# Optimization experiments

Measured on AMD Instinct MI355X. Metric: run time of the kernel, lower is better.

## Reference

```python
import jax, jax.numpy as jnp
import numpy as np

N, E = 50000, 800000
NODE_DIM, EDGE_DIM = 96, 64
IN_DIM = 2 * NODE_DIM + EDGE_DIM  # 256


def setup_inputs() -> dict:
    key = jax.random.key(0)
    k = jax.random.split(key, 7)
    h = jax.random.normal(k[0], (N, NODE_DIM), dtype=jnp.float32)
    edge_index = jax.random.randint(k[1], (2, E), 0, N, dtype=jnp.int64)
    edge_attr = jax.random.normal(k[2], (E, EDGE_DIM), dtype=jnp.float32)
    # Linear params (PyTorch default-ish scale)
    s = 1.0 / np.sqrt(IN_DIM)
    W_e = jax.random.uniform(k[3], (IN_DIM, NODE_DIM), jnp.float32, -s, s)
    b_e = jax.random.uniform(k[4], (NODE_DIM,), jnp.float32, -s, s)
    W_n = jax.random.uniform(k[5], (IN_DIM, NODE_DIM), jnp.float32, -s, s)
    b_n = jax.random.uniform(k[6], (NODE_DIM,), jnp.float32, -s, s)
    return {"h": h, "edge_index": edge_index, "edge_attr": edge_attr,
            "W_e": W_e, "b_e": b_e, "W_n": W_n, "b_n": b_n}


def reference(h, edge_index, edge_attr, W_e, b_e, W_n, b_n):
    src, dst = edge_index[0], edge_index[1]
    concat = jnp.concatenate([h[src], h[dst], edge_attr], axis=-1)  # [E, 256]
    gates = jax.nn.sigmoid(concat @ W_e + b_e)                      # [E, node_dim]
    messages = jax.nn.softplus(concat @ W_n + b_n)                  # [E, node_dim]
    gated = gates * messages
    n = h.shape[0]
    h_new = jax.ops.segment_sum(gated, dst, num_segments=n)         # [N, node_dim]
    edge_count = jax.ops.segment_sum(jnp.ones((dst.shape[0],), h.dtype), dst, num_segments=n)
    edge_count = jnp.clip(edge_count, 1.0, None)[:, None]
    return h + h_new / edge_count
```

## Files before the change

kernel.cpp:

```cpp
#include <hip/hip_runtime.h>
#include <hip/hip_bf16.h>


#define NODE_DIM 96
#define EDGE_DIM 64
#define IN_DIM   256
#define NT_TILES 12
#define KT_TILES 8

typedef float  f32x4  __attribute__((ext_vector_type(4)));
typedef __bf16 bf16x8 __attribute__((ext_vector_type(8)));

__device__ __forceinline__ unsigned short bf16rne(float f) {
    unsigned int u = __float_as_uint(f);
    u += 0x7FFFu + ((u >> 16) & 1u);
    return (unsigned short)(u >> 16);
}

__global__ void pack_w_kernel(const float* __restrict__ We,
                              const float* __restrict__ Wn,
                              unsigned short* __restrict__ bpack) {
    int t = blockIdx.x * blockDim.x + threadIdx.x;
    if (t >= KT_TILES * NT_TILES * 64) return;
    int tile = t >> 6, lane = t & 63;
    int kt = tile / NT_TILES, nt = tile % NT_TILES;
    const float* W = (nt < 6) ? We : Wn;
    int n  = (nt % 6) * 16 + (lane & 15);
    int k0 = kt * 32 + (lane >> 4) * 8;
    union { unsigned short u[8]; uint4 v; } tmp;
#pragma unroll
    for (int j = 0; j < 8; ++j) tmp.u[j] = bf16rne(W[(k0 + j) * NODE_DIM + n]);
    *(uint4*)(bpack + (size_t)t * 8) = tmp.v;
}

__global__ void cvt_h_kernel(const float* __restrict__ h,
                             unsigned short* __restrict__ hb, int total8) {
    int i = blockIdx.x * 256 + threadIdx.x;
    if (i >= total8) return;
    const float4 v0 = ((const float4*)h)[i * 2];
    const float4 v1 = ((const float4*)h)[i * 2 + 1];
    union { unsigned short u[8]; uint4 v; } p;
    p.u[0] = bf16rne(v0.x); p.u[1] = bf16rne(v0.y);
    p.u[2] = bf16rne(v0.z); p.u[3] = bf16rne(v0.w);
    p.u[4] = bf16rne(v1.x); p.u[5] = bf16rne(v1.y);
    p.u[6] = bf16rne(v1.z); p.u[7] = bf16rne(v1.w);
    ((uint4*)hb)[i] = p.v;
}

__global__ void hist_kernel(const int* __restrict__ eidx, unsigned* __restrict__ deg, int E) {
    int e = blockIdx.x * 256 + threadIdx.x;
    if (e < E) atomicAdd(deg + eidx[E + e], 1u);
}

__device__ __forceinline__ unsigned block_excl_scan_256(unsigned v, int tid,
                                                        unsigned* wsum, unsigned* wpre,
                                                        unsigned* total) {
    int lane = tid & 63, w = tid >> 6;
    unsigned inc = v;
#pragma unroll
    for (int o = 1; o < 64; o <<= 1) {
        unsigned t = __shfl_up(inc, o, 64);
        if (lane >= o) inc += t;
    }
    if (lane == 63) wsum[w] = inc;
    __syncthreads();
    if (tid == 0) {
        unsigned s = 0;
#pragma unroll
        for (int k = 0; k < 4; ++k) { wpre[k] = s; s += wsum[k]; }
        *total = s;
    }
    __syncthreads();
    return inc - v + wpre[w];
}

__global__ void scan_block_kernel(const unsigned* __restrict__ deg,
                                  unsigned* __restrict__ scanned,
                                  unsigned* __restrict__ blocksum, int N) {
    __shared__ unsigned wsum[4], wpre[4], total;
    int tid = threadIdx.x;
    int i = blockIdx.x * 256 + tid;
    unsigned v = (i < N) ? deg[i] : 0u;
    unsigned excl = block_excl_scan_256(v, tid, wsum, wpre, &total);
    if (i < N) scanned[i] = excl;
    if (tid == 0) blocksum[blockIdx.x] = total;
}

__global__ void scan_sums_kernel(const unsigned* __restrict__ blocksum,
                                 unsigned* __restrict__ blockpref, int NB) {
    __shared__ unsigned wsum[4], wpre[4], total;
    int tid = threadIdx.x;
    unsigned v = (tid < NB) ? blocksum[tid] : 0u;
    unsigned excl = block_excl_scan_256(v, tid, wsum, wpre, &total);
    if (tid < NB) blockpref[tid] = excl;
}

__global__ void scan_finalize_kernel(const unsigned* __restrict__ scanned,
                                     const unsigned* __restrict__ blockpref,
                                     unsigned* __restrict__ offsets,
                                     unsigned* __restrict__ cursor, int N, int E) {
    int i = blockIdx.x * 256 + threadIdx.x;
    if (i < N) {
        unsigned o = scanned[i] + blockpref[i >> 8];
        offsets[i] = o;
        cursor[i]  = o;
    }
    if (i == 0) offsets[N] = (unsigned)E;
}

__global__ void scatter_kernel(const int* __restrict__ eidx,
                               unsigned* __restrict__ cursor,
                               unsigned* __restrict__ rank, int E) {
    int e = blockIdx.x * 256 + threadIdx.x;
    if (e < E) {
        int d = eidx[E + e];
        rank[e] = atomicAdd(cursor + d, 1u);
    }
}

__global__ __launch_bounds__(256, 2)
void gemm_msg_kernel(const unsigned short* __restrict__ hb,
                     const int*   __restrict__ eidx,
                     const float* __restrict__ ea,
                     const unsigned short* __restrict__ bpack,
                     const float* __restrict__ be,
                     const float* __restrict__ bn,
                     const unsigned* __restrict__ rank,
                     unsigned short* __restrict__ msg,
                     int E) {
    const int tid  = threadIdx.x;
    const int wave = tid >> 6, lane = tid & 63;
    const int m    = lane & 15;
    const int quad = lane >> 4;
    const int base = blockIdx.x * 128 + wave * 32;

    const unsigned short* hsq[2];
    const unsigned short* hdq[2];
    const float*          epq[2];
#pragma unroll
    for (int mt = 0; mt < 2; ++mt) {
        int e  = base + mt * 16 + m;
        int eg = (e < E) ? e : (E - 1);
        int src = eidx[eg];
        int dst = eidx[E + eg];
        hsq[mt] = hb + (size_t)src * NODE_DIM + quad * 8;
        hdq[mt] = hb + (size_t)dst * NODE_DIM + quad * 8;
        epq[mt] = ea + (size_t)eg  * EDGE_DIM + quad * 8;
    }

    unsigned prow_[2][4];
#pragma unroll
    for (int mt = 0; mt < 2; ++mt)
#pragma unroll
        for (int r = 0; r < 4; ++r) {
            int ee = base + mt * 16 + quad * 4 + r;
            prow_[mt][r] = rank[(ee < E) ? ee : (E - 1)];
        }

    float bev[6], bnv[6];
#pragma unroll
    for (int nt = 0; nt < 6; ++nt) {
        bev[nt] = be[nt * 16 + m];
        bnv[nt] = bn[nt * 16 + m];
    }

    bf16x8 A[2][KT_TILES];
#pragma unroll
    for (int mt = 0; mt < 2; ++mt) {
#pragma unroll
        for (int kt = 0; kt < 3; ++kt)
            A[mt][kt] = *(const bf16x8*)(hsq[mt] + kt * 32);
#pragma unroll
        for (int kt = 3; kt < 6; ++kt)
            A[mt][kt] = *(const bf16x8*)(hdq[mt] + (kt - 3) * 32);
#pragma unroll
        for (int kt = 6; kt < 8; ++kt) {
            const float4 v0 = *(const float4*)(epq[mt] + (kt - 6) * 32);
            const float4 v1 = *(const float4*)(epq[mt] + (kt - 6) * 32 + 4);
            union { unsigned short u[8]; bf16x8 b; } t;
            t.u[0] = bf16rne(v0.x); t.u[1] = bf16rne(v0.y);
            t.u[2] = bf16rne(v0.z); t.u[3] = bf16rne(v0.w);
            t.u[4] = bf16rne(v1.x); t.u[5] = bf16rne(v1.y);
            t.u[6] = bf16rne(v1.z); t.u[7] = bf16rne(v1.w);
            A[mt][kt] = t.b;
        }
    }

    f32x4 acc[2][NT_TILES];
#pragma unroll
    for (int mt = 0; mt < 2; ++mt)
#pragma unroll
        for (int nt = 0; nt < NT_TILES; ++nt) acc[mt][nt] = (f32x4){0.f, 0.f, 0.f, 0.f};

    const unsigned short* bl = bpack + lane * 8;
#pragma unroll
    for (int kt = 0; kt < KT_TILES; ++kt) {
        bf16x8 Bf[NT_TILES];
#pragma unroll
        for (int nt = 0; nt < NT_TILES; ++nt)
            Bf[nt] = *(const bf16x8*)(bl + (kt * NT_TILES + nt) * 512);
#pragma unroll
        for (int nt = 0; nt < NT_TILES; ++nt) {
            acc[0][nt] = __builtin_amdgcn_mfma_f32_16x16x32_bf16(A[0][kt], Bf[nt], acc[0][nt], 0, 0, 0);
            acc[1][nt] = __builtin_amdgcn_mfma_f32_16x16x32_bf16(A[1][kt], Bf[nt], acc[1][nt], 0, 0, 0);
        }
    }

    const float LOG2E = 1.44269504f, LN2 = 0.69314718f;
#pragma unroll
    for (int mt = 0; mt < 2; ++mt) {
#pragma unroll
        for (int r = 0; r < 4; ++r) {
            const int ee = base + mt * 16 + quad * 4 + r;
            if (ee >= E) continue;
            const size_t prow = (size_t)prow_[mt][r] * NODE_DIM;
#pragma unroll
            for (int nt = 0; nt < 6; ++nt) {
                const int col = nt * 16 + m;
                float g  = acc[mt][nt][r]     + bev[nt];
                float mm = acc[mt][nt + 6][r] + bnv[nt];
                float eg_  = __builtin_amdgcn_exp2f(-g * LOG2E);
                float gate = __builtin_amdgcn_rcpf(1.0f + eg_);
                float ae   = __builtin_amdgcn_exp2f(-fabsf(mm) * LOG2E);
                float sp   = fmaxf(mm, 0.0f) + LN2 * __builtin_amdgcn_logf(1.0f + ae);
                msg[prow + col] = bf16rne(gate * sp);
            }
        }
    }
}

__global__ __launch_bounds__(256)
void aggregate_kernel(const float* __restrict__ h,
                      const unsigned* __restrict__ offsets,
                      const unsigned short* __restrict__ msg,
                      float* __restrict__ out, int N) {
    int t = blockIdx.x * 256 + threadIdx.x;
    int n = t / 12, g = t % 12;
    if (n >= N) return;

    const unsigned o0 = offsets[n];
    const unsigned o1 = offsets[n + 1];
    const int deg = (int)(o1 - o0);

    float s0 = 0.f, s1 = 0.f, s2 = 0.f, s3 = 0.f;
    float s4 = 0.f, s5 = 0.f, s6 = 0.f, s7 = 0.f;
    for (unsigned k = o0; k < o1; ++k) {
        const uint4 v = *(const uint4*)(msg + (size_t)k * NODE_DIM + g * 8);
        s0 += __uint_as_float((v.x & 0xFFFFu) << 16);
        s1 += __uint_as_float(v.x & 0xFFFF0000u);
        s2 += __uint_as_float((v.y & 0xFFFFu) << 16);
        s3 += __uint_as_float(v.y & 0xFFFF0000u);
        s4 += __uint_as_float((v.z & 0xFFFFu) << 16);
        s5 += __uint_as_float(v.z & 0xFFFF0000u);
        s6 += __uint_as_float((v.w & 0xFFFFu) << 16);
        s7 += __uint_as_float(v.w & 0xFFFF0000u);
    }
    const float inv = 1.0f / (float)((deg > 0) ? deg : 1);
    const size_t basei = (size_t)n * NODE_DIM + g * 8;
    const float4 h0 = *(const float4*)(h + basei);
    const float4 h1 = *(const float4*)(h + basei + 4);
    float4 o0v = {h0.x + s0 * inv, h0.y + s1 * inv, h0.z + s2 * inv, h0.w + s3 * inv};
    float4 o1v = {h1.x + s4 * inv, h1.y + s5 * inv, h1.z + s6 * inv, h1.w + s7 * inv};
    *(float4*)(out + basei)     = o0v;
    *(float4*)(out + basei + 4) = o1v;
}

#define TILE_E 64
__global__ __launch_bounds__(256, 4)
void cgconv_atomic_kernel(const float* __restrict__ h,
                          const int*   __restrict__ eidx,
                          const float* __restrict__ ea,
                          const unsigned short* __restrict__ bpack,
                          const float* __restrict__ be,
                          const float* __restrict__ bn,
                          float* __restrict__ hnew,
                          float* __restrict__ cnt,
                          int E) {
    const int tid  = threadIdx.x;
    const int wave = tid >> 6, lane = tid & 63;
    const int m    = lane & 15;
    const int quad = lane >> 4;

    const int e  = blockIdx.x * TILE_E + wave * 16 + m;
    const int eg = (e < E) ? e : (E - 1);
    const int src = eidx[eg];
    const int dst = eidx[E + eg];
    if (quad == 0 && e < E) unsafeAtomicAdd(cnt + dst, 1.0f);

    f32x4 acc[NT_TILES];
#pragma unroll
    for (int nt = 0; nt < NT_TILES; ++nt) acc[nt] = (f32x4){0.f, 0.f, 0.f, 0.f};

    const float* hsrc = h + (size_t)src * NODE_DIM;
    const float* hdst = h + (size_t)dst * NODE_DIM;
    const float* earo = ea + (size_t)eg * EDGE_DIM;

#pragma unroll
    for (int kt = 0; kt < KT_TILES; ++kt) {
        const int ko = kt * 32 + quad * 8;
        const float* p;
        if (kt < 3)      p = hsrc + ko;
        else if (kt < 6) p = hdst + (ko - NODE_DIM);
        else             p = earo + (ko - 2 * NODE_DIM);
        const float4 v0 = *(const float4*)p;
        const float4 v1 = *(const float4*)(p + 4);
        union { unsigned short u[8]; bf16x8 b; } A;
        A.u[0] = bf16rne(v0.x); A.u[1] = bf16rne(v0.y);
        A.u[2] = bf16rne(v0.z); A.u[3] = bf16rne(v0.w);
        A.u[4] = bf16rne(v1.x); A.u[5] = bf16rne(v1.y);
        A.u[6] = bf16rne(v1.z); A.u[7] = bf16rne(v1.w);
#pragma unroll
        for (int nt = 0; nt < NT_TILES; ++nt) {
            bf16x8 bfrag = *(const bf16x8*)(bpack +
                             (size_t)((kt * NT_TILES + nt) * 64 + lane) * 8);
            acc[nt] = __builtin_amdgcn_mfma_f32_16x16x32_bf16(A.b, bfrag, acc[nt], 0, 0, 0);
        }
    }

    int drow[4], erow[4];
#pragma unroll
    for (int r = 0; r < 4; ++r) {
        drow[r] = __shfl(dst, quad * 4 + r, 64);
        erow[r] = blockIdx.x * TILE_E + wave * 16 + quad * 4 + r;
    }
#pragma unroll
    for (int nt = 0; nt < 6; ++nt) {
        const int col = nt * 16 + m;
        const float bev = be[col];
        const float bnv = bn[col];
#pragma unroll
        for (int r = 0; r < 4; ++r) {
            if (erow[r] >= E) continue;
            float g  = acc[nt][r] + bev;
            float mm = acc[nt + 6][r] + bnv;
            float gate = 1.0f / (1.0f + __expf(-g));
            float sp   = fmaxf(mm, 0.0f) + __logf(1.0f + __expf(-fabsf(mm)));
            unsafeAtomicAdd(hnew + (size_t)drow[r] * NODE_DIM + col, gate * sp);
        }
    }
}

__global__ void finalize_kernel(const float* __restrict__ h,
                                const float* __restrict__ hnew,
                                const float* __restrict__ cnt,
                                float* __restrict__ out,
                                int total4) {
    int i = blockIdx.x * blockDim.x + threadIdx.x;
    if (i >= total4) return;
    int n = i / 24;
    float inv = 1.0f / fmaxf(cnt[n], 1.0f);
    float4 hv = ((const float4*)h)[i];
    float4 av = ((const float4*)hnew)[i];
    float4 o = {hv.x + av.x * inv, hv.y + av.y * inv, hv.z + av.z * inv, hv.w + av.w * inv};
    ((float4*)out)[i] = o;
}

extern "C" void kernel_launch(void* const* d_in, const int* in_sizes, int n_in,
                              void* d_out, int out_size, void* d_ws, size_t ws_size,
                              hipStream_t stream) {
    const float* h   = (const float*)d_in[0];
    const int*   ei  = (const int*)  d_in[1];
    const float* ea  = (const float*)d_in[2];
    const float* We  = (const float*)d_in[3];
    const float* be  = (const float*)d_in[4];
    const float* Wn  = (const float*)d_in[5];
    const float* bn  = (const float*)d_in[6];

    const int N = in_sizes[0] / NODE_DIM;
    const int E = in_sizes[2] / EDGE_DIM;
    char* ws = (char*)d_ws;

    size_t off = 0;
    auto take = [&](size_t bytes) { size_t o = off; off = (off + bytes + 511) & ~(size_t)511; return o; };
    const size_t O_BPACK  = take((size_t)KT_TILES * NT_TILES * 64 * 16);
    const size_t O_DEG    = take((size_t)N * 4);
    const size_t O_SCAN   = take((size_t)N * 4);
    const size_t O_BSUM   = take(1024);
    const size_t O_BPREF  = take(1024);
    const size_t O_OFFS   = take((size_t)(N + 1) * 4);
    const size_t O_CURS   = take((size_t)N * 4);
    const size_t O_RANK   = take((size_t)E * 4);
    const size_t O_HB     = take((size_t)N * NODE_DIM * 2);
    const size_t O_MSG    = take((size_t)E * NODE_DIM * 2);
    const size_t NEED = off;

    unsigned short* bpack = (unsigned short*)(ws + O_BPACK);
    pack_w_kernel<<<(KT_TILES * NT_TILES * 64 + 255) / 256, 256, 0, stream>>>(We, Wn, bpack);

    if (ws_size >= NEED) {
        unsigned* deg    = (unsigned*)(ws + O_DEG);
        unsigned* scn    = (unsigned*)(ws + O_SCAN);
        unsigned* bsum   = (unsigned*)(ws + O_BSUM);
        unsigned* bpref  = (unsigned*)(ws + O_BPREF);
        unsigned* offs   = (unsigned*)(ws + O_OFFS);
        unsigned* curs   = (unsigned*)(ws + O_CURS);
        unsigned* rank   = (unsigned*)(ws + O_RANK);
        unsigned short* hb  = (unsigned short*)(ws + O_HB);
        unsigned short* msg = (unsigned short*)(ws + O_MSG);

        hipMemsetAsync(deg, 0, (size_t)N * 4, stream);

        const int total8 = N * NODE_DIM / 8;
        cvt_h_kernel<<<(total8 + 255) / 256, 256, 0, stream>>>(h, hb, total8);

        const int NB = (N + 255) / 256;
        hist_kernel<<<(E + 255) / 256, 256, 0, stream>>>(ei, deg, E);
        scan_block_kernel<<<NB, 256, 0, stream>>>(deg, scn, bsum, N);
        scan_sums_kernel<<<1, 256, 0, stream>>>(bsum, bpref, NB);
        scan_finalize_kernel<<<NB, 256, 0, stream>>>(scn, bpref, offs, curs, N, E);
        scatter_kernel<<<(E + 255) / 256, 256, 0, stream>>>(ei, curs, rank, E);

        gemm_msg_kernel<<<(E + 127) / 128, 256, 0, stream>>>(hb, ei, ea, bpack, be, bn, rank, msg, E);

        const int aggthreads = N * 12;
        aggregate_kernel<<<(aggthreads + 255) / 256, 256, 0, stream>>>(h, offs, msg, (float*)d_out, N);
    } else {
        size_t cnt_off  = O_DEG;
        size_t hnew_off = (cnt_off + (size_t)N * 4 + 511) & ~(size_t)511;
        float* cnt  = (float*)(ws + cnt_off);
        float* hnew = (float*)(ws + hnew_off);
        hipMemsetAsync(ws + cnt_off, 0, hnew_off - cnt_off + (size_t)N * NODE_DIM * 4, stream);
        cgconv_atomic_kernel<<<(E + TILE_E - 1) / TILE_E, 256, 0, stream>>>(
            h, ei, ea, bpack, be, bn, hnew, cnt, E);
        const int total4 = N * (NODE_DIM / 4);
        finalize_kernel<<<(total4 + 255) / 256, 256, 0, stream>>>(h, hnew, cnt, (float*)d_out, total4);
    }
}
```

Baseline: 616.3 us.

## Fuse prep kernels, merge scan stages, and split GEMM N across wave pairs

Weight packing, the h-to-bf16 conversion and the degree histogram now run in a single prep kernel. The block-prefix scan kernel is removed, and each finalize block sums the preceding block totals itself. The message GEMM now assigns 64 edges to each pair of waves, and each wave computes half of the output columns for 4 M-tiles. This cuts launch overhead and accumulator register pressure, and loads A fragments per k-step instead of holding all of them. In exchange, A (gathered h rows) is loaded redundantly by both waves of a pair, and the finalize blocks repeat the prefix summation.

```diff
diff --git a/kernel.cpp b/kernel.cpp
--- a/kernel.cpp
+++ b/kernel.cpp
@@ -7,6 +7,7 @@
 #define IN_DIM   256
 #define NT_TILES 12
 #define KT_TILES 8
+#define PACK_TOTAL (KT_TILES * NT_TILES * 64)
 
 typedef float  f32x4  __attribute__((ext_vector_type(4)));
 typedef __bf16 bf16x8 __attribute__((ext_vector_type(8)));
@@ -17,11 +18,43 @@
     return (unsigned short)(u >> 16);
 }
 
+__global__ void prep_kernel(const float* __restrict__ We,
+                            const float* __restrict__ Wn,
+                            unsigned short* __restrict__ bpack,
+                            const float* __restrict__ h,
+                            unsigned short* __restrict__ hb, int total8,
+                            const int* __restrict__ eidx,
+                            unsigned* __restrict__ deg, int E) {
+    int t = blockIdx.x * 256 + threadIdx.x;
+    if (t < PACK_TOTAL) {
+        int tile = t >> 6, lane = t & 63;
+        int kt = tile / NT_TILES, nt = tile % NT_TILES;
+        const float* W = (nt < 6) ? We : Wn;
+        int n  = (nt % 6) * 16 + (lane & 15);
+        int k0 = kt * 32 + (lane >> 4) * 8;
+        union { unsigned short u[8]; uint4 v; } tmp;
+#pragma unroll
+        for (int j = 0; j < 8; ++j) tmp.u[j] = bf16rne(W[(k0 + j) * NODE_DIM + n]);
+        *(uint4*)(bpack + (size_t)t * 8) = tmp.v;
+    }
+    if (t < total8) {
+        const float4 v0 = ((const float4*)h)[t * 2];
+        const float4 v1 = ((const float4*)h)[t * 2 + 1];
+        union { unsigned short u[8]; uint4 v; } p;
+        p.u[0] = bf16rne(v0.x); p.u[1] = bf16rne(v0.y);
+        p.u[2] = bf16rne(v0.z); p.u[3] = bf16rne(v0.w);
+        p.u[4] = bf16rne(v1.x); p.u[5] = bf16rne(v1.y);
+        p.u[6] = bf16rne(v1.z); p.u[7] = bf16rne(v1.w);
+        ((uint4*)hb)[t] = p.v;
+    }
+    if (t < E) atomicAdd(deg + eidx[E + t], 1u);
+}
+
 __global__ void pack_w_kernel(const float* __restrict__ We,
                               const float* __restrict__ Wn,
                               unsigned short* __restrict__ bpack) {
     int t = blockIdx.x * blockDim.x + threadIdx.x;
-    if (t >= KT_TILES * NT_TILES * 64) return;
+    if (t >= PACK_TOTAL) return;
     int tile = t >> 6, lane = t & 63;
     int kt = tile / NT_TILES, nt = tile % NT_TILES;
     const float* W = (nt < 6) ? We : Wn;
@@ -31,25 +64,6 @@
 #pragma unroll
     for (int j = 0; j < 8; ++j) tmp.u[j] = bf16rne(W[(k0 + j) * NODE_DIM + n]);
     *(uint4*)(bpack + (size_t)t * 8) = tmp.v;
-}
-
-__global__ void cvt_h_kernel(const float* __restrict__ h,
-                             unsigned short* __restrict__ hb, int total8) {
-    int i = blockIdx.x * 256 + threadIdx.x;
-    if (i >= total8) return;
-    const float4 v0 = ((const float4*)h)[i * 2];
-    const float4 v1 = ((const float4*)h)[i * 2 + 1];
-    union { unsigned short u[8]; uint4 v; } p;
-    p.u[0] = bf16rne(v0.x); p.u[1] = bf16rne(v0.y);
-    p.u[2] = bf16rne(v0.z); p.u[3] = bf16rne(v0.w);
-    p.u[4] = bf16rne(v1.x); p.u[5] = bf16rne(v1.y);
-    p.u[6] = bf16rne(v1.z); p.u[7] = bf16rne(v1.w);
-    ((uint4*)hb)[i] = p.v;
-}
-
-__global__ void hist_kernel(const int* __restrict__ eidx, unsigned* __restrict__ deg, int E) {
-    int e = blockIdx.x * 256 + threadIdx.x;
-    if (e < E) atomicAdd(deg + eidx[E + e], 1u);
 }
 
 __device__ __forceinline__ unsigned block_excl_scan_256(unsigned v, int tid,
@@ -86,22 +100,24 @@
     if (tid == 0) blocksum[blockIdx.x] = total;
 }
 
-__global__ void scan_sums_kernel(const unsigned* __restrict__ blocksum,
-                                 unsigned* __restrict__ blockpref, int NB) {
-    __shared__ unsigned wsum[4], wpre[4], total;
-    int tid = threadIdx.x;
-    unsigned v = (tid < NB) ? blocksum[tid] : 0u;
-    unsigned excl = block_excl_scan_256(v, tid, wsum, wpre, &total);
-    if (tid < NB) blockpref[tid] = excl;
-}
-
-__global__ void scan_finalize_kernel(const unsigned* __restrict__ scanned,
-                                     const unsigned* __restrict__ blockpref,
-                                     unsigned* __restrict__ offsets,
-                                     unsigned* __restrict__ cursor, int N, int E) {
-    int i = blockIdx.x * 256 + threadIdx.x;
+__global__ void scan_finalize2_kernel(const unsigned* __restrict__ scanned,
+                                      const unsigned* __restrict__ blocksum,
+                                      unsigned* __restrict__ offsets,
+                                      unsigned* __restrict__ cursor,
+                                      int N, int E, int NB) {
+    __shared__ unsigned wtot[4];
+    const int tid = threadIdx.x, bid = blockIdx.x;
+    const int lane = tid & 63, w = tid >> 6;
+    unsigned v = 0;
+    for (int j = tid; j < bid; j += 256) v += blocksum[j];
+#pragma unroll
+    for (int o = 1; o < 64; o <<= 1) v += __shfl_xor(v, o, 64);
+    if (lane == 0) wtot[w] = v;
+    __syncthreads();
+    const unsigned bpref = wtot[0] + wtot[1] + wtot[2] + wtot[3];
+    const int i = bid * 256 + tid;
     if (i < N) {
-        unsigned o = scanned[i] + blockpref[i >> 8];
+        unsigned o = scanned[i] + bpref;
         offsets[i] = o;
         cursor[i]  = o;
     }
@@ -130,15 +146,17 @@
                      int E) {
     const int tid  = threadIdx.x;
     const int wave = tid >> 6, lane = tid & 63;
+    const int wp   = wave >> 1;
+    const int half = wave & 1;
     const int m    = lane & 15;
     const int quad = lane >> 4;
-    const int base = blockIdx.x * 128 + wave * 32;
-
-    const unsigned short* hsq[2];
-    const unsigned short* hdq[2];
-    const float*          epq[2];
-#pragma unroll
-    for (int mt = 0; mt < 2; ++mt) {
+    const int base = blockIdx.x * 128 + wp * 64;
+
+    const unsigned short* hsq[4];
+    const unsigned short* hdq[4];
+    const float*          epq[4];
+#pragma unroll
+    for (int mt = 0; mt < 4; ++mt) {
         int e  = base + mt * 16 + m;
         int eg = (e < E) ? e : (E - 1);
         int src = eidx[eg];
@@ -148,77 +166,80 @@
         epq[mt] = ea + (size_t)eg  * EDGE_DIM + quad * 8;
     }
 
-    unsigned prow_[2][4];
-#pragma unroll
-    for (int mt = 0; mt < 2; ++mt)
+    unsigned prow_[4][4];
+#pragma unroll
+    for (int mt = 0; mt < 4; ++mt)
 #pragma unroll
         for (int r = 0; r < 4; ++r) {
             int ee = base + mt * 16 + quad * 4 + r;
             prow_[mt][r] = rank[(ee < E) ? ee : (E - 1)];
         }
 
-    float bev[6], bnv[6];
-#pragma unroll
-    for (int nt = 0; nt < 6; ++nt) {
-        bev[nt] = be[nt * 16 + m];
-        bnv[nt] = bn[nt * 16 + m];
-    }
-
-    bf16x8 A[2][KT_TILES];
-#pragma unroll
-    for (int mt = 0; mt < 2; ++mt) {
-#pragma unroll
-        for (int kt = 0; kt < 3; ++kt)
-            A[mt][kt] = *(const bf16x8*)(hsq[mt] + kt * 32);
-#pragma unroll
-        for (int kt = 3; kt < 6; ++kt)
-            A[mt][kt] = *(const bf16x8*)(hdq[mt] + (kt - 3) * 32);
-#pragma unroll
-        for (int kt = 6; kt < 8; ++kt) {
-            const float4 v0 = *(const float4*)(epq[mt] + (kt - 6) * 32);
-            const float4 v1 = *(const float4*)(epq[mt] + (kt - 6) * 32 + 4);
-            union { unsigned short u[8]; bf16x8 b; } t;
-            t.u[0] = bf16rne(v0.x); t.u[1] = bf16rne(v0.y);
-            t.u[2] = bf16rne(v0.z); t.u[3] = bf16rne(v0.w);
-            t.u[4] = bf16rne(v1.x); t.u[5] = bf16rne(v1.y);
-            t.u[6] = bf16rne(v1.z); t.u[7] = bf16rne(v1.w);
-            A[mt][kt] = t.b;
-        }
-    }
-
-    f32x4 acc[2][NT_TILES];
-#pragma unroll
-    for (int mt = 0; mt < 2; ++mt)
-#pragma unroll
-        for (int nt = 0; nt < NT_TILES; ++nt) acc[mt][nt] = (f32x4){0.f, 0.f, 0.f, 0.f};
+    float bev[3], bnv[3];
+#pragma unroll
+    for (int p = 0; p < 3; ++p) {
+        bev[p] = be[half * 48 + p * 16 + m];
+        bnv[p] = bn[half * 48 + p * 16 + m];
+    }
+
+    f32x4 accg[4][3], accm[4][3];
+#pragma unroll
+    for (int mt = 0; mt < 4; ++mt)
+#pragma unroll
+        for (int p = 0; p < 3; ++p) {
+            accg[mt][p] = (f32x4){0.f, 0.f, 0.f, 0.f};
+            accm[mt][p] = (f32x4){0.f, 0.f, 0.f, 0.f};
+        }
 
     const unsigned short* bl = bpack + lane * 8;
 #pragma unroll
     for (int kt = 0; kt < KT_TILES; ++kt) {
-        bf16x8 Bf[NT_TILES];
-#pragma unroll
-        for (int nt = 0; nt < NT_TILES; ++nt)
-            Bf[nt] = *(const bf16x8*)(bl + (kt * NT_TILES + nt) * 512);
-#pragma unroll
-        for (int nt = 0; nt < NT_TILES; ++nt) {
-            acc[0][nt] = __builtin_amdgcn_mfma_f32_16x16x32_bf16(A[0][kt], Bf[nt], acc[0][nt], 0, 0, 0);
-            acc[1][nt] = __builtin_amdgcn_mfma_f32_16x16x32_bf16(A[1][kt], Bf[nt], acc[1][nt], 0, 0, 0);
-        }
+        bf16x8 Bg[3], Bm[3];
+#pragma unroll
+        for (int p = 0; p < 3; ++p) {
+            Bg[p] = *(const bf16x8*)(bl + (kt * NT_TILES + half * 3 + p) * 512);
+            Bm[p] = *(const bf16x8*)(bl + (kt * NT_TILES + 6 + half * 3 + p) * 512);
+        }
+        bf16x8 A[4];
+#pragma unroll
+        for (int mt = 0; mt < 4; ++mt) {
+            if (kt < 3) {
+                A[mt] = *(const bf16x8*)(hsq[mt] + kt * 32);
+            } else if (kt < 6) {
+                A[mt] = *(const bf16x8*)(hdq[mt] + (kt - 3) * 32);
+            } else {
+                const float4 v0 = *(const float4*)(epq[mt] + (kt - 6) * 32);
+                const float4 v1 = *(const float4*)(epq[mt] + (kt - 6) * 32 + 4);
+                union { unsigned short u[8]; bf16x8 b; } t;
+                t.u[0] = bf16rne(v0.x); t.u[1] = bf16rne(v0.y);
+                t.u[2] = bf16rne(v0.z); t.u[3] = bf16rne(v0.w);
+                t.u[4] = bf16rne(v1.x); t.u[5] = bf16rne(v1.y);
+                t.u[6] = bf16rne(v1.z); t.u[7] = bf16rne(v1.w);
+                A[mt] = t.b;
+            }
+        }
+#pragma unroll
+        for (int p = 0; p < 3; ++p)
+#pragma unroll
+            for (int mt = 0; mt < 4; ++mt) {
+                accg[mt][p] = __builtin_amdgcn_mfma_f32_16x16x32_bf16(A[mt], Bg[p], accg[mt][p], 0, 0, 0);
+                accm[mt][p] = __builtin_amdgcn_mfma_f32_16x16x32_bf16(A[mt], Bm[p], accm[mt][p], 0, 0, 0);
+            }
     }
 
     const float LOG2E = 1.44269504f, LN2 = 0.69314718f;
 #pragma unroll
-    for (int mt = 0; mt < 2; ++mt) {
+    for (int mt = 0; mt < 4; ++mt) {
 #pragma unroll
         for (int r = 0; r < 4; ++r) {
             const int ee = base + mt * 16 + quad * 4 + r;
             if (ee >= E) continue;
             const size_t prow = (size_t)prow_[mt][r] * NODE_DIM;
 #pragma unroll
-            for (int nt = 0; nt < 6; ++nt) {
-                const int col = nt * 16 + m;
-                float g  = acc[mt][nt][r]     + bev[nt];
-                float mm = acc[mt][nt + 6][r] + bnv[nt];
+            for (int p = 0; p < 3; ++p) {
+                const int col = half * 48 + p * 16 + m;
+                float g  = accg[mt][p][r] + bev[p];
+                float mm = accm[mt][p][r] + bnv[p];
                 float eg_  = __builtin_amdgcn_exp2f(-g * LOG2E);
                 float gate = __builtin_amdgcn_rcpf(1.0f + eg_);
                 float ae   = __builtin_amdgcn_exp2f(-fabsf(mm) * LOG2E);
@@ -372,11 +393,10 @@
 
     size_t off = 0;
     auto take = [&](size_t bytes) { size_t o = off; off = (off + bytes + 511) & ~(size_t)511; return o; };
-    const size_t O_BPACK  = take((size_t)KT_TILES * NT_TILES * 64 * 16);
+    const size_t O_BPACK  = take((size_t)PACK_TOTAL * 16);
     const size_t O_DEG    = take((size_t)N * 4);
     const size_t O_SCAN   = take((size_t)N * 4);
-    const size_t O_BSUM   = take(1024);
-    const size_t O_BPREF  = take(1024);
+    const size_t O_BSUM   = take(4096);
     const size_t O_OFFS   = take((size_t)(N + 1) * 4);
     const size_t O_CURS   = take((size_t)N * 4);
     const size_t O_RANK   = take((size_t)E * 4);
@@ -385,13 +405,11 @@
     const size_t NEED = off;
 
     unsigned short* bpack = (unsigned short*)(ws + O_BPACK);
-    pack_w_kernel<<<(KT_TILES * NT_TILES * 64 + 255) / 256, 256, 0, stream>>>(We, Wn, bpack);
 
     if (ws_size >= NEED) {
         unsigned* deg    = (unsigned*)(ws + O_DEG);
         unsigned* scn    = (unsigned*)(ws + O_SCAN);
         unsigned* bsum   = (unsigned*)(ws + O_BSUM);
-        unsigned* bpref  = (unsigned*)(ws + O_BPREF);
         unsigned* offs   = (unsigned*)(ws + O_OFFS);
         unsigned* curs   = (unsigned*)(ws + O_CURS);
         unsigned* rank   = (unsigned*)(ws + O_RANK);
@@ -401,13 +419,16 @@
         hipMemsetAsync(deg, 0, (size_t)N * 4, stream);
 
         const int total8 = N * NODE_DIM / 8;
-        cvt_h_kernel<<<(total8 + 255) / 256, 256, 0, stream>>>(h, hb, total8);
-
         const int NB = (N + 255) / 256;
-        hist_kernel<<<(E + 255) / 256, 256, 0, stream>>>(ei, deg, E);
+
+        int prep_threads = E;
+        if (total8 > prep_threads) prep_threads = total8;
+        if (PACK_TOTAL > prep_threads) prep_threads = PACK_TOTAL;
+        prep_kernel<<<(prep_threads + 255) / 256, 256, 0, stream>>>(
+            We, Wn, bpack, h, hb, total8, ei, deg, E);
+
         scan_block_kernel<<<NB, 256, 0, stream>>>(deg, scn, bsum, N);
-        scan_sums_kernel<<<1, 256, 0, stream>>>(bsum, bpref, NB);
-        scan_finalize_kernel<<<NB, 256, 0, stream>>>(scn, bpref, offs, curs, N, E);
+        scan_finalize2_kernel<<<NB, 256, 0, stream>>>(scn, bsum, offs, curs, N, E, NB);
         scatter_kernel<<<(E + 255) / 256, 256, 0, stream>>>(ei, curs, rank, E);
 
         gemm_msg_kernel<<<(E + 127) / 128, 256, 0, stream>>>(hb, ei, ea, bpack, be, bn, rank, msg, E);
@@ -415,6 +436,7 @@
         const int aggthreads = N * 12;
         aggregate_kernel<<<(aggthreads + 255) / 256, 256, 0, stream>>>(h, offs, msg, (float*)d_out, N);
     } else {
+        pack_w_kernel<<<(PACK_TOTAL + 255) / 256, 256, 0, stream>>>(We, Wn, bpack);
         size_t cnt_off  = O_DEG;
         size_t hnew_off = (cnt_off + (size_t)N * 4 + 511) & ~(size_t)511;
         float* cnt  = (float*)(ws + cnt_off);
```

Measured after the change: 604.9 us. Within noise of the previous version (-1.9%).
